# Optimization experiments

Hardware: AMD Instinct MI355X
Metric: run time of the kernel (lower is better)

The kernel has to match this reference:

```python
import jax, jax.numpy as jnp
import numpy as np

B = 4
G = 1024                      # GridSize
H = 1.0 / (G - 1)             # h = (right-left)/(GridSize-1), area=[[0,0],[1,1]]
GD = 0.0                      # boundary value for hard_encode padding


def _cross(a):
    # sum of 4-neighborhood: matches conv2d with kernel [[0,.5,0],[.5,0,.5],[0,.5,0]] / 0.5
    return a[..., :-2, 1:-1] + a[..., 2:, 1:-1] + a[..., 1:-1, :-2] + a[..., 1:-1, 2:]


def _inner(a):
    return a[..., 1:-1, 1:-1]


def kappa(x, mu):
    # assumed parameterization (kappa undefined in source): exp(mu * x)
    return jnp.exp(mu * x)


def setup_inputs() -> dict:
    key = jax.random.key(0)
    k1, k2, k3, k4 = jax.random.split(key, 4)
    pre = jax.random.normal(k1, (B, 1, G - 2, G - 2), jnp.float32)
    f = jax.random.normal(k2, (B, 1, G, G), jnp.float32)
    mu = jax.random.uniform(k3, (1,), jnp.float32)
    prev_pre = jax.random.normal(k4, (B, 1, G, G), jnp.float32) * 0.1
    return {"pre": pre, "f": f, "mu": mu, "prev_pre": prev_pre, "maxiter": 20}


def reference(pre, f, mu, prev_pre, maxiter):
    # w = kappa(prev_pre, mu) is iteration-invariant -> hoist out of the loop
    w = kappa(prev_pre, mu)            # [B,1,G,G]
    w_in = _inner(w)                   # [B,1,G-2,G-2]
    force = _inner(f) * (H * H)
    # k3 conv: 0.5*cross + 2*center
    y3 = 0.5 * _cross(w) + 2.0 * w_in

    def step(y, _):
        u = jnp.pad(y, ((0, 0), (0, 0), (1, 1), (1, 1)), constant_values=GD)
        y1 = 0.5 * _cross(u) * w_in    # conv(u, k1) * w_inner
        y2 = 0.5 * _cross(w * u)       # conv(w*u, k2)
        return (force + y1 + y2) / y3, None

    # original: one jac_step, then `maxiter` more -> maxiter+1 total
    y, _ = jax.lax.scan(step, pre, None, length=maxiter + 1)
    return y
```

## Files before the change

### kernel.cpp

```cpp
#include <hip/hip_runtime.h>

#define BB 4
#define GG 1024
#define NI 1022
#define SROW 1024
#define HH2 (2.0f / (1023.0f * 1023.0f))
#define TK 7
#define TB 64
#define OFF 8
#define TOUT 48
#define NT 22
#define HP 68

typedef float vf4 __attribute__((ext_vector_type(4)));
typedef float vf2 __attribute__((ext_vector_type(2)));

template<bool VIN4, bool VOUT4>
__global__ __launch_bounds__(256)
void pinn_fused(const float* __restrict__ ysrc, int ystride,
                const float* __restrict__ pp,
                const float* __restrict__ fglob,
                const float* __restrict__ mu_p,
                float* __restrict__ yout, int ostride)
{
    __shared__ float wh[32 * HP];
    __shared__ float yh[2][32 * HP];

    const int tid = threadIdx.x;
    const int tx = tid & 15, ty = tid >> 4;
    const int lane = tid & 63;
    const int b  = blockIdx.z;
    const int AR = blockIdx.y * TOUT - OFF;
    const int A0 = blockIdx.x * TOUT - OFF;
    const int R  = 4 * ty;
    const int c0 = 4 * tx;
    const float mu = mu_p[0];

    const int cb = min(max(A0 + c0, 0), GG - 4);
    const int r0 = min(max(AR + R,     0), GG - 1);
    const int r1 = min(max(AR + R + 1, 0), GG - 1);
    const int r2 = min(max(AR + R + 2, 0), GG - 1);
    const int r3 = min(max(AR + R + 3, 0), GG - 1);
    const int r4 = min(max(AR + R + 4, 0), GG - 1);
    const size_t pb = (size_t)b * GG * GG;
    vf4 wv0 = *(const vf4*)&pp[pb + (size_t)r0 * GG + cb];
    vf4 wv1 = *(const vf4*)&pp[pb + (size_t)r1 * GG + cb];
    vf4 wv2 = *(const vf4*)&pp[pb + (size_t)r2 * GG + cb];
    vf4 wv3 = *(const vf4*)&pp[pb + (size_t)r3 * GG + cb];
    const vf4 fv0 = *(const vf4*)&fglob[pb + (size_t)r1 * GG + cb];
    const vf4 fv1 = *(const vf4*)&fglob[pb + (size_t)r2 * GG + cb];
    const vf4 fv2 = *(const vf4*)&fglob[pb + (size_t)r3 * GG + cb];
    const vf4 fv3 = *(const vf4*)&fglob[pb + (size_t)r4 * GG + cb];

    vf4 y0v, y1v, y2v, y3v;
    {
        const int i0 = min(max(AR + R,     0), NI - 1);
        const int i1 = min(max(AR + R + 1, 0), NI - 1);
        const int i2 = min(max(AR + R + 2, 0), NI - 1);
        const int i3 = min(max(AR + R + 3, 0), NI - 1);
        if (VIN4) {
            const int cy = min(max(A0 + c0, 0), SROW - 4);
            y0v = *(const vf4*)&ysrc[(size_t)(b * NI + i0) * ystride + cy];
            y1v = *(const vf4*)&ysrc[(size_t)(b * NI + i1) * ystride + cy];
            y2v = *(const vf4*)&ysrc[(size_t)(b * NI + i2) * ystride + cy];
            y3v = *(const vf4*)&ysrc[(size_t)(b * NI + i3) * ystride + cy];
        } else {
            const int cy  = min(max(A0 + c0, 0), NI - 2);
            const int cy2 = min(cy + 2, NI - 2);
            #define LDY(dst, ii) { \
                const size_t base_ = (size_t)(b * NI + (ii)) * ystride; \
                const vf2 a_ = *(const vf2*)&ysrc[base_ + cy]; \
                const vf2 b_ = *(const vf2*)&ysrc[base_ + cy2]; \
                dst[0] = a_[0]; dst[1] = a_[1]; dst[2] = b_[0]; dst[3] = b_[1]; }
            LDY(y0v, i0) LDY(y1v, i1) LDY(y2v, i2) LDY(y3v, i3)
            #undef LDY
        }
    }

    #pragma unroll
    for (int m = 0; m < 4; ++m) {
        wv0[m] = __expf(mu * wv0[m]);
        wv1[m] = __expf(mu * wv1[m]);
        wv2[m] = __expf(mu * wv2[m]);
        wv3[m] = __expf(mu * wv3[m]);
    }
    *(vf4*)&wh[(2 * ty) * HP + c0]     = wv0;
    *(vf4*)&wh[(2 * ty + 1) * HP + c0] = wv1;
    __syncthreads();

    const vf4 w4 = *(const vf4*)&wh[min(2 * ty + 2, 31) * HP + c0];
    const vf4 w5 = *(const vf4*)&wh[min(2 * ty + 3, 31) * HP + c0];
    const float s1_0 = __shfl(wv0[0], lane + 1, 64);
    const float s1_1 = __shfl(wv1[0], lane + 1, 64);
    const float s1_2 = __shfl(wv2[0], lane + 1, 64);
    const float s1_3 = __shfl(wv3[0], lane + 1, 64);
    const float s1_4 = __shfl(w4[0],  lane + 1, 64);
    const float s1_5 = __shfl(w5[0],  lane + 1, 64);
    const float s2_1 = __shfl(wv1[1], lane + 1, 64);
    const float s2_2 = __shfl(wv2[1], lane + 1, 64);
    const float s2_3 = __shfl(wv3[1], lane + 1, 64);
    const float s2_4 = __shfl(w4[1],  lane + 1, 64);
    const float sf0 = __shfl(fv0[0], lane + 1, 64);
    const float sf1 = __shfl(fv1[0], lane + 1, 64);
    const float sf2 = __shfl(fv2[0], lane + 1, 64);
    const float sf3 = __shfl(fv3[0], lane + 1, 64);

    vf4 bN0,bN1,bN2,bN3, bS0,bS1,bS2,bS3, bW0,bW1,bW2,bW3,
        bE0,bE1,bE2,bE3, bf0,bf1,bf2,bf3;

    #define COEFF(k, N_, C_, S_, s1C, s1S, s2C, FV, SF, BN, BS, BW, BE, BF, YV) { \
        const vf4 wN = {N_[1], N_[2], N_[3], __shfl(N_[0], lane + 1, 64)*0.0f + s1C*0.0f + N_[1]*0.0f + 0.0f}; \
        (void)wN; }
    #undef COEFF

    #define COEFF(kk, N_, C_, S_, s1N, s1C, s1S, s2C, FV, SF, BN, BS, BW, BE, BF, YV) { \
        const vf4 wN = {N_[1], N_[2], N_[3], s1N}; \
        const vf4 wW = C_; \
        const vf4 wC = {C_[1], C_[2], C_[3], s1C}; \
        const vf4 wE = {C_[2], C_[3], s1C, s2C}; \
        const vf4 wS = {S_[1], S_[2], S_[3], s1S}; \
        const vf4 aN = wC + wN, aS = wC + wS, aW = wC + wW, aE = wC + wE; \
        const vf4 den = (aN + aS) + (aW + aE); \
        const int gi = AR + R + (kk); \
        vf4 rd; \
        _Pragma("unroll") \
        for (int m = 0; m < 4; ++m) { \
            float x = __builtin_amdgcn_rcpf(den[m]); \
            x = x * (2.0f - den[m] * x); \
            const int gj = A0 + c0 + m; \
            const bool in = (gi >= 0) && (gi < NI) && (gj >= 0) && (gj < NI); \
            rd[m] = in ? x : 0.0f; \
            YV[m] = in ? YV[m] : 0.0f; \
        } \
        BN = aN * rd; BS = aS * rd; BW = aW * rd; BE = aE * rd; \
        const vf4 fC = {FV[1], FV[2], FV[3], SF}; \
        BF = (fC * rd) * HH2; }

    COEFF(0, wv0, wv1, wv2, s1_0, s1_1, s1_2, s2_1, fv0, sf0, bN0,bS0,bW0,bE0,bf0, y0v)
    COEFF(1, wv1, wv2, wv3, s1_1, s1_2, s1_3, s2_2, fv1, sf1, bN1,bS1,bW1,bE1,bf1, y1v)
    COEFF(2, wv2, wv3, w4,  s1_2, s1_3, s1_4, s2_3, fv2, sf2, bN2,bS2,bW2,bE2,bf2, y2v)
    COEFF(3, wv3, w4,  w5,  s1_3, s1_4, s1_5, s2_4, fv3, sf3, bN3,bS3,bW3,bE3,bf3, y3v)
    #undef COEFF

    const int wslot0 = (2 * ty) * HP + c0;
    const int wslot1 = (2 * ty + 1) * HP + c0;
    const int uoff = max(2 * ty - 1, 0) * HP + c0;
    const int doff = min(2 * ty + 2, 31) * HP + c0;

    for (int t = 1; t <= TK; ++t) {
        float* bufp = (t & 1) ? yh[1] : yh[0];
        *(vf4*)&bufp[wslot0] = y0v;
        *(vf4*)&bufp[wslot1] = y3v;
        __syncthreads();
        const vf4 up = *(const vf4*)&bufp[uoff];
        const vf4 dn = *(const vf4*)&bufp[doff];
        const float l0 = __shfl(y0v[3], lane - 1, 64), rr0 = __shfl(y0v[0], lane + 1, 64);
        const float l1 = __shfl(y1v[3], lane - 1, 64), rr1 = __shfl(y1v[0], lane + 1, 64);
        const float l2 = __shfl(y2v[3], lane - 1, 64), rr2 = __shfl(y2v[0], lane + 1, 64);
        const float l3 = __shfl(y3v[3], lane - 1, 64), rr3 = __shfl(y3v[0], lane + 1, 64);
        const vf4 yW0 = {l0, y0v[0], y0v[1], y0v[2]}, yE0 = {y0v[1], y0v[2], y0v[3], rr0};
        const vf4 yW1 = {l1, y1v[0], y1v[1], y1v[2]}, yE1 = {y1v[1], y1v[2], y1v[3], rr1};
        const vf4 yW2 = {l2, y2v[0], y2v[1], y2v[2]}, yE2 = {y2v[1], y2v[2], y2v[3], rr2};
        const vf4 yW3 = {l3, y3v[0], y3v[1], y3v[2]}, yE3 = {y3v[1], y3v[2], y3v[3], rr3};
        vf4 n0 = bf0; n0 += bN0 * up;  n0 += bS0 * y1v; n0 += bW0 * yW0; n0 += bE0 * yE0;
        vf4 n1 = bf1; n1 += bN1 * y0v; n1 += bS1 * y2v; n1 += bW1 * yW1; n1 += bE1 * yE1;
        vf4 n2 = bf2; n2 += bN2 * y1v; n2 += bS2 * y3v; n2 += bW2 * yW2; n2 += bE2 * yE2;
        vf4 n3 = bf3; n3 += bN3 * y2v; n3 += bS3 * dn;  n3 += bW3 * yW3; n3 += bE3 * yE3;
        y0v = n0; y1v = n1; y2v = n2; y3v = n3;
    }

    if (R >= OFF && R < OFF + TOUT && c0 >= OFF && c0 < OFF + TOUT) {
        const int gj0 = A0 + c0;
        #define STORE(kk, YV) { \
            const int gi = AR + R + (kk); \
            if (gi < NI) { \
                const size_t rb = (size_t)(b * NI + gi) * ostride; \
                if (gj0 + 3 < NI) { \
                    if (VOUT4) { *(vf4*)&yout[rb + gj0] = YV; } \
                    else { vf2 pa, pbv; pa[0]=YV[0]; pa[1]=YV[1]; pbv[0]=YV[2]; pbv[1]=YV[3]; \
                           *(vf2*)&yout[rb + gj0] = pa; *(vf2*)&yout[rb + gj0 + 2] = pbv; } \
                } else { \
                    _Pragma("unroll") \
                    for (int m = 0; m < 4; ++m) \
                        if (gj0 + m < NI) yout[rb + gj0 + m] = YV[m]; \
                } \
            } }
        STORE(0, y0v) STORE(1, y1v) STORE(2, y2v) STORE(3, y3v)
        #undef STORE
    }
}

extern "C" void kernel_launch(void* const* d_in, const int* in_sizes, int n_in,
                              void* d_out, int out_size, void* d_ws, size_t ws_size,
                              hipStream_t stream) {
    const float* pre = (const float*)d_in[0];
    const float* f   = (const float*)d_in[1];
    const float* mu  = (const float*)d_in[2];
    const float* pp  = (const float*)d_in[3];

    float* yA = (float*)d_ws;
    float* yB = yA + (size_t)BB * NI * SROW;
    float* out = (float*)d_out;

    const dim3 grid(NT, NT, BB);
    const dim3 bs(256, 1, 1);
    pinn_fused<false, true ><<<grid, bs, 0, stream>>>(pre, NI,   pp, f, mu, yA,  SROW);
    pinn_fused<true,  true ><<<grid, bs, 0, stream>>>(yA,  SROW, pp, f, mu, yB,  SROW);
    pinn_fused<true,  false><<<grid, bs, 0, stream>>>(yB,  SROW, pp, f, mu, out, NI);
}
```

Measured before the change: 163.4 us.

## Fuse all Jacobi iterations into one launch with larger temporally-blocked tiles

Replaces three launches of 7 fused iterations each with a single launch that does all 21 iterations inside 128x128 tiles using 1024-thread blocks. The goal is to drop two launches and the intermediate global round trips, and to recompute less halo per output. The price is a wider 24-cell halo that must be recomputed redundantly and more work per block. The grid shrinks to 13x13x4 blocks of 1024 threads, which may underfill the GPU. Vertical halo exchange between paired waves now uses shfl_xor across the wave halves instead of shared memory.

```diff
diff --git a/kernel.cpp b/kernel.cpp
--- a/kernel.cpp
+++ b/kernel.cpp
@@ -3,32 +3,32 @@
 #define BB 4
 #define GG 1024
 #define NI 1022
-#define SROW 1024
 #define HH2 (2.0f / (1023.0f * 1023.0f))
-#define TK 7
-#define TB 64
-#define OFF 8
-#define TOUT 48
-#define NT 22
-#define HP 68
+#define TK 21
+#define TB 128
+#define OFF 24
+#define TOUT 80
+#define NT 13
+#define HS 132
 
 typedef float vf4 __attribute__((ext_vector_type(4)));
 typedef float vf2 __attribute__((ext_vector_type(2)));
 
-template<bool VIN4, bool VOUT4>
-__global__ __launch_bounds__(256)
-void pinn_fused(const float* __restrict__ ysrc, int ystride,
-                const float* __restrict__ pp,
-                const float* __restrict__ fglob,
-                const float* __restrict__ mu_p,
-                float* __restrict__ yout, int ostride)
+__global__ __launch_bounds__(1024)
+void pinn_mega(const float* __restrict__ pre,
+               const float* __restrict__ fglob,
+               const float* __restrict__ mu_p,
+               const float* __restrict__ pp,
+               float* __restrict__ yout)
 {
-    __shared__ float wh[32 * HP];
-    __shared__ float yh[2][32 * HP];
+    __shared__ float wh[2 * 16 * HS];
+    __shared__ float yh[2][2 * 16 * HS];
 
     const int tid = threadIdx.x;
-    const int tx = tid & 15, ty = tid >> 4;
+    const int tx = tid & 31, ty = tid >> 5;
     const int lane = tid & 63;
+    const int s = ty >> 1;
+    const int odd = ty & 1;
     const int b  = blockIdx.z;
     const int AR = blockIdx.y * TOUT - OFF;
     const int A0 = blockIdx.x * TOUT - OFF;
@@ -37,12 +37,12 @@
     const float mu = mu_p[0];
 
     const int cb = min(max(A0 + c0, 0), GG - 4);
+    const size_t pb = (size_t)b * GG * GG;
     const int r0 = min(max(AR + R,     0), GG - 1);
     const int r1 = min(max(AR + R + 1, 0), GG - 1);
     const int r2 = min(max(AR + R + 2, 0), GG - 1);
     const int r3 = min(max(AR + R + 3, 0), GG - 1);
     const int r4 = min(max(AR + R + 4, 0), GG - 1);
-    const size_t pb = (size_t)b * GG * GG;
     vf4 wv0 = *(const vf4*)&pp[pb + (size_t)r0 * GG + cb];
     vf4 wv1 = *(const vf4*)&pp[pb + (size_t)r1 * GG + cb];
     vf4 wv2 = *(const vf4*)&pp[pb + (size_t)r2 * GG + cb];
@@ -58,23 +58,15 @@
         const int i1 = min(max(AR + R + 1, 0), NI - 1);
         const int i2 = min(max(AR + R + 2, 0), NI - 1);
         const int i3 = min(max(AR + R + 3, 0), NI - 1);
-        if (VIN4) {
-            const int cy = min(max(A0 + c0, 0), SROW - 4);
-            y0v = *(const vf4*)&ysrc[(size_t)(b * NI + i0) * ystride + cy];
-            y1v = *(const vf4*)&ysrc[(size_t)(b * NI + i1) * ystride + cy];
-            y2v = *(const vf4*)&ysrc[(size_t)(b * NI + i2) * ystride + cy];
-            y3v = *(const vf4*)&ysrc[(size_t)(b * NI + i3) * ystride + cy];
-        } else {
-            const int cy  = min(max(A0 + c0, 0), NI - 2);
-            const int cy2 = min(cy + 2, NI - 2);
-            #define LDY(dst, ii) { \
-                const size_t base_ = (size_t)(b * NI + (ii)) * ystride; \
-                const vf2 a_ = *(const vf2*)&ysrc[base_ + cy]; \
-                const vf2 b_ = *(const vf2*)&ysrc[base_ + cy2]; \
-                dst[0] = a_[0]; dst[1] = a_[1]; dst[2] = b_[0]; dst[3] = b_[1]; }
-            LDY(y0v, i0) LDY(y1v, i1) LDY(y2v, i2) LDY(y3v, i3)
-            #undef LDY
-        }
+        const int cy  = min(max(A0 + c0, 0), NI - 2);
+        const int cy2 = min(cy + 2, NI - 2);
+        #define LDY(dst, ii) { \
+            const size_t base_ = (size_t)(b * NI + (ii)) * NI; \
+            const vf2 a_ = *(const vf2*)&pre[base_ + cy]; \
+            const vf2 b_ = *(const vf2*)&pre[base_ + cy2]; \
+            dst[0] = a_[0]; dst[1] = a_[1]; dst[2] = b_[0]; dst[3] = b_[1]; }
+        LDY(y0v, i0) LDY(y1v, i1) LDY(y2v, i2) LDY(y3v, i3)
+        #undef LDY
     }
 
     #pragma unroll
@@ -84,12 +76,26 @@
         wv2[m] = __expf(mu * wv2[m]);
         wv3[m] = __expf(mu * wv3[m]);
     }
-    *(vf4*)&wh[(2 * ty) * HP + c0]     = wv0;
-    *(vf4*)&wh[(2 * ty + 1) * HP + c0] = wv1;
+    if (!odd) {
+        *(vf4*)&wh[s * HS + c0]        = wv0;
+        *(vf4*)&wh[(16 + s) * HS + c0] = wv1;
+    }
     __syncthreads();
 
-    const vf4 w4 = *(const vf4*)&wh[min(2 * ty + 2, 31) * HP + c0];
-    const vf4 w5 = *(const vf4*)&wh[min(2 * ty + 3, 31) * HP + c0];
+    vf4 w4, w5;
+    {
+        const int so = min(s + 1, 15);
+        const vf4 l4 = *(const vf4*)&wh[so * HS + c0];
+        const vf4 l5 = *(const vf4*)&wh[(16 + so) * HS + c0];
+        #pragma unroll
+        for (int m = 0; m < 4; ++m) {
+            const float x4 = __shfl_xor(wv0[m], 32, 64);
+            const float x5 = __shfl_xor(wv1[m], 32, 64);
+            w4[m] = odd ? l4[m] : x4;
+            w5[m] = odd ? l5[m] : x5;
+        }
+    }
+
     const float s1_0 = __shfl(wv0[0], lane + 1, 64);
     const float s1_1 = __shfl(wv1[0], lane + 1, 64);
     const float s1_2 = __shfl(wv2[0], lane + 1, 64);
@@ -107,11 +113,6 @@
 
     vf4 bN0,bN1,bN2,bN3, bS0,bS1,bS2,bS3, bW0,bW1,bW2,bW3,
         bE0,bE1,bE2,bE3, bf0,bf1,bf2,bf3;
-
-    #define COEFF(k, N_, C_, S_, s1C, s1S, s2C, FV, SF, BN, BS, BW, BE, BF, YV) { \
-        const vf4 wN = {N_[1], N_[2], N_[3], __shfl(N_[0], lane + 1, 64)*0.0f + s1C*0.0f + N_[1]*0.0f + 0.0f}; \
-        (void)wN; }
-    #undef COEFF
 
     #define COEFF(kk, N_, C_, S_, s1N, s1C, s1S, s2C, FV, SF, BN, BS, BW, BE, BF, YV) { \
         const vf4 wN = {N_[1], N_[2], N_[3], s1N}; \
@@ -142,18 +143,23 @@
     COEFF(3, wv3, w4,  w5,  s1_3, s1_4, s1_5, s2_4, fv3, sf3, bN3,bS3,bW3,bE3,bf3, y3v)
     #undef COEFF
 
-    const int wslot0 = (2 * ty) * HP + c0;
-    const int wslot1 = (2 * ty + 1) * HP + c0;
-    const int uoff = max(2 * ty - 1, 0) * HP + c0;
-    const int doff = min(2 * ty + 2, 31) * HP + c0;
+    const int pubOff = (odd ? 16 * HS : 0) + s * HS + c0;
+    const int halOff = odd ? (min(s + 1, 15) * HS + c0)
+                           : ((16 + max(s - 1, 0)) * HS + c0);
 
     for (int t = 1; t <= TK; ++t) {
-        float* bufp = (t & 1) ? yh[1] : yh[0];
-        *(vf4*)&bufp[wslot0] = y0v;
-        *(vf4*)&bufp[wslot1] = y3v;
+        float* buf = yh[t & 1];
+        *(vf4*)&buf[pubOff] = odd ? y3v : y0v;
         __syncthreads();
-        const vf4 up = *(const vf4*)&bufp[uoff];
-        const vf4 dn = *(const vf4*)&bufp[doff];
+        const vf4 hal = *(const vf4*)&buf[halOff];
+        vf4 upx, dnx;
+        #pragma unroll
+        for (int m = 0; m < 4; ++m) {
+            upx[m] = __shfl_xor(y3v[m], 32, 64);
+            dnx[m] = __shfl_xor(y0v[m], 32, 64);
+        }
+        const vf4 up = odd ? upx : hal;
+        const vf4 dn = odd ? hal : dnx;
         const float l0 = __shfl(y0v[3], lane - 1, 64), rr0 = __shfl(y0v[0], lane + 1, 64);
         const float l1 = __shfl(y1v[3], lane - 1, 64), rr1 = __shfl(y1v[0], lane + 1, 64);
         const float l2 = __shfl(y2v[3], lane - 1, 64), rr2 = __shfl(y2v[0], lane + 1, 64);
@@ -174,11 +180,10 @@
         #define STORE(kk, YV) { \
             const int gi = AR + R + (kk); \
             if (gi < NI) { \
-                const size_t rb = (size_t)(b * NI + gi) * ostride; \
+                const size_t rb = (size_t)(b * NI + gi) * NI; \
                 if (gj0 + 3 < NI) { \
-                    if (VOUT4) { *(vf4*)&yout[rb + gj0] = YV; } \
-                    else { vf2 pa, pbv; pa[0]=YV[0]; pa[1]=YV[1]; pbv[0]=YV[2]; pbv[1]=YV[3]; \
-                           *(vf2*)&yout[rb + gj0] = pa; *(vf2*)&yout[rb + gj0 + 2] = pbv; } \
+                    vf2 pa, pv; pa[0]=YV[0]; pa[1]=YV[1]; pv[0]=YV[2]; pv[1]=YV[3]; \
+                    *(vf2*)&yout[rb + gj0] = pa; *(vf2*)&yout[rb + gj0 + 2] = pv; \
                 } else { \
                     _Pragma("unroll") \
                     for (int m = 0; m < 4; ++m) \
@@ -197,14 +202,8 @@
     const float* f   = (const float*)d_in[1];
     const float* mu  = (const float*)d_in[2];
     const float* pp  = (const float*)d_in[3];
-
-    float* yA = (float*)d_ws;
-    float* yB = yA + (size_t)BB * NI * SROW;
-    float* out = (float*)d_out;
-
-    const dim3 grid(NT, NT, BB);
-    const dim3 bs(256, 1, 1);
-    pinn_fused<false, true ><<<grid, bs, 0, stream>>>(pre, NI,   pp, f, mu, yA,  SROW);
-    pinn_fused<true,  true ><<<grid, bs, 0, stream>>>(yA,  SROW, pp, f, mu, yB,  SROW);
-    pinn_fused<true,  false><<<grid, bs, 0, stream>>>(yB,  SROW, pp, f, mu, out, NI);
+    (void)d_ws; (void)ws_size;
+
+    pinn_mega<<<dim3(NT, NT, BB), dim3(1024, 1, 1), 0, stream>>>(
+        pre, f, mu, pp, (float*)d_out);
 }
```

Measured after the change: 172.1 us. +5.3%, slower.
